# Kernel optimization log

Measured on AMD Instinct MI355X. Metric: run time of the kernel, lower is better.

Reference implementation:

```python
import jax, jax.numpy as jnp
import numpy as np
import math

B, N, CS = 1, 2048, 384
H, C, PQK, PV = 12, 16, 4, 8
INF, EPS = 100000.0, 1e-08


def setup_inputs() -> dict:
    key = jax.random.key(0)
    ks = jax.random.split(key, 16)
    hc = H * C
    hpq = H * PQK * 3
    hpkv = H * (PQK + PV) * 3
    cod = H * (C + 4 * PV)
    sc = 0.02
    return {
        "s": jax.random.normal(ks[0], (B, N, CS), jnp.float32),
        "rot": jax.random.normal(ks[1], (B, N, 3, 3), jnp.float32),
        "trans": jax.random.normal(ks[2], (B, N, 3), jnp.float32),
        "mask": jnp.ones((B, N), jnp.float32),
        "Wq": jax.random.normal(ks[3], (hc, CS), jnp.float32) * sc,
        "bq": jnp.zeros((hc,), jnp.float32),
        "Wkv": jax.random.normal(ks[4], (2 * hc, CS), jnp.float32) * sc,
        "bkv": jnp.zeros((2 * hc,), jnp.float32),
        "Wqp": jax.random.normal(ks[5], (hpq, CS), jnp.float32) * sc,
        "bqp": jnp.zeros((hpq,), jnp.float32),
        "Wkvp": jax.random.normal(ks[6], (hpkv, CS), jnp.float32) * sc,
        "bkvp": jnp.zeros((hpkv,), jnp.float32),
        "head_weights": jnp.full((H,), 0.541324854612918, jnp.float32),
        "Wout": jax.random.normal(ks[7], (CS, H * cod // H), jnp.float32) * sc,
        "bout": jnp.zeros((CS,), jnp.float32),
    }


def _points(s, W, b, rot, trans, npts):
    # torch.split into 3 chunks of H*npts then stack at -1 -> [B,N,H*npts,3]
    p = jnp.einsum("bni,oi->bno", s, W) + b
    p = jnp.moveaxis(p.reshape(B, N, 3, H * npts), -2, -1)  # [B,N,H*npts,3]
    p = jnp.einsum("bnij,bnmj->bnmi", rot, p) + trans[:, :, None, :]  # rigid apply
    return p.reshape(B, N, H, npts, 3)


def reference(s, rot, trans, mask, Wq, bq, Wkv, bkv, Wqp, bqp, Wkvp, bkvp, head_weights, Wout, bout):
    q = (jnp.einsum("bni,oi->bno", s, Wq) + bq).reshape(B, N, H, C)
    kv = (jnp.einsum("bni,oi->bno", s, Wkv) + bkv).reshape(B, N, H, 2 * C)
    k, v = kv[..., :C], kv[..., C:]

    q_pts = _points(s, Wqp, bqp, rot, trans, PQK)             # [B,N,H,PQK,3]
    kv_pts = _points(s, Wkvp, bkvp, rot, trans, PQK + PV)
    k_pts, v_pts = kv_pts[..., :PQK, :], kv_pts[..., PQK:, :]  # [B,N,H,PQK,3], [B,N,H,PV,3]

    a = jnp.einsum("bihc,bjhc->bhij", q, k) * math.sqrt(1.0 / (3 * C))

    # sum_{p,c} |q_pts_i - k_pts_j|^2 via norm expansion (avoids [N,N,P,3])
    q2 = jnp.moveaxis(jnp.sum(q_pts ** 2, axis=(-1, -2)), -1, 1)  # [B,H,N]
    k2 = jnp.moveaxis(jnp.sum(k_pts ** 2, axis=(-1, -2)), -1, 1)
    cross = jnp.einsum("bihpc,bjhpc->bhij", q_pts, k_pts)
    d2 = q2[..., :, None] + k2[..., None, :] - 2.0 * cross       # [B,H,N,N]

    hw = jax.nn.softplus(head_weights) * math.sqrt(1.0 / (3 * (PQK * 9.0 / 2)))
    pt_att = -0.5 * hw[None, :, None, None] * d2

    sq_mask = INF * (mask[:, None, :, None] * mask[:, None, None, :] - 1.0)  # [B,1,N,N]
    a = jax.nn.softmax(a + pt_att + sq_mask, axis=-1)

    o = jnp.einsum("bhij,bjhc->bihc", a, v).reshape(B, N, H * C)
    o_pt = jnp.einsum("bhij,bjhpc->bihpc", a, v_pts)             # [B,N,H,PV,3]
    o_pt = jnp.einsum("bnji,bnhpj->bnhpi", rot, o_pt - trans[:, :, None, None, :])  # invert_apply

    dists = jnp.sqrt(jnp.sum(o_pt ** 2, axis=-1) + EPS).reshape(B, N, H * PV)
    o_pt_f = o_pt.reshape(B, N, H * PV, 3)
    feats = jnp.concatenate([o, o_pt_f[..., 0], o_pt_f[..., 1], o_pt_f[..., 2], dists], axis=-1)
    return jnp.einsum("bnf,of->bno", feats, Wout) + bout
```

## Files before the change

### kernel.cpp

```cpp
#include <hip/hip_runtime.h>
#include <hip/hip_bf16.h>
#include <cstdint>
#include <cstddef>

#define Hh    12
#define Nseq  2048
#define PSTR  1152
#define EPSm  1e-8f
#define MASKV 1024.0f

typedef unsigned short ushort_t;
typedef __attribute__((ext_vector_type(8))) short bf8_t;
typedef __attribute__((ext_vector_type(4))) short s4_t;
typedef __attribute__((ext_vector_type(4))) float f4_t;

#define OFF_PALL   0
#define OFF_WALLB  2359296
#define OFF_BALL   2580480
#define OFF_SB     2581632
#define OFF_WOUTB  2974848
#define OFF_FEATSB 3085440
#define OFF_AU     3675264
#define OFF_KU     4068480
#define OFF_VU     4461696
#define WS_FLOATS  5051520

__device__ __forceinline__ ushort_t bfr(float x) {
    union { float f; uint32_t u; } v; v.f = x;
    uint32_t r = v.u + 0x7FFFu + ((v.u >> 16) & 1u);
    return (ushort_t)(r >> 16);
}

__global__ __launch_bounds__(256) void prep(
    const float* __restrict__ s, const float* __restrict__ Wout,
    const float* __restrict__ Wq, const float* __restrict__ Wkv,
    const float* __restrict__ Wqp, const float* __restrict__ Wkvp,
    const float* __restrict__ bq, const float* __restrict__ bkv,
    const float* __restrict__ bqp, const float* __restrict__ bkvp,
    ushort_t* __restrict__ Wallb, float* __restrict__ ball,
    ushort_t* __restrict__ sb, ushort_t* __restrict__ Woutb)
{
    int idx = blockIdx.x * 256 + threadIdx.x;
    if (idx < 1152 * 384) {
        int r = idx / 384, c = idx % 384;
        float v;
        if (r < 192)      v = Wq [(size_t)r * 384 + c];
        else if (r < 576) v = Wkv[(size_t)(r - 192) * 384 + c];
        else if (r < 720) v = Wqp[(size_t)(r - 576) * 384 + c];
        else              v = Wkvp[(size_t)(r - 720) * 384 + c];
        Wallb[idx] = bfr(v);
    }
    if (idx < 1152) {
        float v;
        if (idx < 192)      v = bq[idx];
        else if (idx < 576) v = bkv[idx - 192];
        else if (idx < 720) v = bqp[idx - 576];
        else                v = bkvp[idx - 720];
        ball[idx] = v;
    }
    if (idx < 2048 * 384) sb[idx] = bfr(s[idx]);
    if (idx < 384 * 576)  Woutb[idx] = bfr(Wout[idx]);
}

template<int BM, int BN>
__global__ __launch_bounds__(256) void gemm_mfma(
    const ushort_t* __restrict__ A, const ushort_t* __restrict__ W,
    const float* __restrict__ bias, float* __restrict__ C,
    int M, int Nn, int K)
{
    constexpr int WM = BM / 2, WN = BN / 2;
    constexpr int MI = WM / 16, NJ = WN / 16;
    __shared__ ushort_t As[BM][40];
    __shared__ ushort_t Bs[BN][40];

    const int bm = blockIdx.y * BM;
    const int bn = blockIdx.x * BN;
    const int t  = threadIdx.x;
    const int w  = t >> 6, lane = t & 63;
    const int m  = lane & 15, quad = lane >> 4;
    const int wm = (w >> 1) * WM, wn = (w & 1) * WN;

    f4_t acc[MI][NJ];
    #pragma unroll
    for (int i2 = 0; i2 < MI; ++i2)
        #pragma unroll
        for (int j2 = 0; j2 < NJ; ++j2)
            acc[i2][j2] = (f4_t){0.f, 0.f, 0.f, 0.f};

    for (int k0 = 0; k0 < K; k0 += 32) {
        #pragma unroll
        for (int u = 0; u < BM / 64; ++u) {
            int e = t + u * 256;
            int r = e >> 2, kk = (e & 3) * 8;
            *(uint4*)&As[r][kk] = *(const uint4*)&A[(size_t)(bm + r) * K + k0 + kk];
        }
        #pragma unroll
        for (int u = 0; u < BN / 64; ++u) {
            int e = t + u * 256;
            int r = e >> 2, kk = (e & 3) * 8;
            *(uint4*)&Bs[r][kk] = *(const uint4*)&W[(size_t)(bn + r) * K + k0 + kk];
        }
        __syncthreads();
        bf8_t af[MI], bfv[NJ];
        #pragma unroll
        for (int x = 0; x < MI; ++x) af[x]  = *(const bf8_t*)&As[wm + x * 16 + m][quad * 8];
        #pragma unroll
        for (int x = 0; x < NJ; ++x) bfv[x] = *(const bf8_t*)&Bs[wn + x * 16 + m][quad * 8];
        #pragma unroll
        for (int i2 = 0; i2 < MI; ++i2)
            #pragma unroll
            for (int j2 = 0; j2 < NJ; ++j2)
                acc[i2][j2] = __builtin_amdgcn_mfma_f32_16x16x32_bf16(
                    af[i2], bfv[j2], acc[i2][j2], 0, 0, 0);
        __syncthreads();
    }

    #pragma unroll
    for (int j2 = 0; j2 < NJ; ++j2) {
        int col = bn + wn + j2 * 16 + m;
        float bb = bias[col];
        #pragma unroll
        for (int i2 = 0; i2 < MI; ++i2)
            #pragma unroll
            for (int r = 0; r < 4; ++r) {
                int row = bm + wm + i2 * 16 + quad * 4 + r;
                C[(size_t)row * Nn + col] = acc[i2][j2][r] + bb;
            }
    }
}

__global__ __launch_bounds__(128) void pack_aug(
    const float* __restrict__ Pall, const float* __restrict__ rot,
    const float* __restrict__ trans, const float* __restrict__ mask,
    const float* __restrict__ hwv,
    ushort_t* __restrict__ AU, ushort_t* __restrict__ KU,
    ushort_t* __restrict__ VU)
{
    __shared__ float S[8][1156];
    const int n0 = blockIdx.x * 8;
    const int t  = threadIdx.x;

    #pragma unroll
    for (int u = 0; u < 18; ++u) {
        int f = t + u * 128;
        int rr = f / 288, c4 = f % 288;
        float4 v = *(const float4*)&Pall[(size_t)(n0 + rr) * PSTR + c4 * 4];
        *(float4*)&S[rr][c4 * 4] = v;
    }
    __syncthreads();

    if (t >= 96) return;
    const int nl = t & 7, h = t >> 3;
    const int n  = n0 + nl;
    const float* row = S[nl];

    const float whw = 0.5f * logf(1.0f + expf(hwv[h])) * 0.13608276348795434f;
    const float scale_a = 0.14433756729740643f;

    float R[9], T[3];
    #pragma unroll
    for (int z = 0; z < 9; ++z) R[z] = rot[(size_t)n * 9 + z];
    #pragma unroll
    for (int d = 0; d < 3; ++d) T[d] = trans[(size_t)n * 3 + d];

    float qpv[12], q2 = 0.f;
    #pragma unroll
    for (int p = 0; p < 4; ++p) {
        float r0 = row[576 +   0 + h * 4 + p];
        float r1 = row[576 +  48 + h * 4 + p];
        float r2 = row[576 +  96 + h * 4 + p];
        #pragma unroll
        for (int d = 0; d < 3; ++d) {
            float o = R[d*3+0]*r0 + R[d*3+1]*r1 + R[d*3+2]*r2 + T[d];
            qpv[p * 3 + d] = o;
            q2 += o * o;
        }
    }

    float kpv[12], vpv[24], k2 = 0.f;
    #pragma unroll
    for (int pt = 0; pt < 12; ++pt) {
        float r0 = row[720 +   0 + h * 12 + pt];
        float r1 = row[720 + 144 + h * 12 + pt];
        float r2 = row[720 + 288 + h * 12 + pt];
        #pragma unroll
        for (int d = 0; d < 3; ++d) {
            float o = R[d*3+0]*r0 + R[d*3+1]*r1 + R[d*3+2]*r2 + T[d];
            if (pt < 4) { kpv[pt * 3 + d] = o; k2 += o * o; }
            else        { vpv[(pt - 4) * 3 + d] = o; }
        }
    }

    const float mi = mask[n];

    __align__(16) ushort_t a32[32];
    #pragma unroll
    for (int c = 0; c < 16; ++c) a32[c] = bfr(row[h * 16 + c] * scale_a);
    #pragma unroll
    for (int z = 0; z < 12; ++z) a32[16 + z] = bfr(qpv[z] * (2.0f * whw));
    a32[28] = bfr(-whw);
    a32[29] = bfr(-whw * q2);
    a32[30] = bfr(mi * MASKV);
    a32[31] = bfr(-MASKV);
    ushort_t* adst = AU + ((size_t)h * Nseq + n) * 32;
    #pragma unroll
    for (int u = 0; u < 4; ++u) ((uint4*)adst)[u] = ((const uint4*)a32)[u];

    const float* kvrow = row + 192 + h * 32;
    __align__(16) ushort_t k32[32];
    #pragma unroll
    for (int c = 0; c < 16; ++c) k32[c] = bfr(kvrow[c]);
    #pragma unroll
    for (int z = 0; z < 12; ++z) k32[16 + z] = bfr(kpv[z]);
    k32[28] = bfr(k2);
    k32[29] = 0x3F80;
    k32[30] = bfr(mi);
    k32[31] = 0x3F80;
    ushort_t* kdst = KU + ((size_t)h * Nseq + n) * 32;
    #pragma unroll
    for (int u = 0; u < 4; ++u) ((uint4*)kdst)[u] = ((const uint4*)k32)[u];

    ushort_t* vb = VU + (size_t)h * 98304 + (size_t)(n >> 5) * 1536 + (n & 31);
    #pragma unroll
    for (int c = 0; c < 16; ++c) vb[c * 32] = bfr(kvrow[16 + c]);
    #pragma unroll
    for (int z = 0; z < 24; ++z) vb[(16 + z) * 32] = bfr(vpv[z]);
    vb[40 * 32] = 0x3F80;
    #pragma unroll
    for (int c = 41; c < 48; ++c) vb[c * 32] = 0;
}

__device__ __forceinline__ bf8_t expack(f4_t s) {
    s4_t p;
    p[0] = (short)bfr(__expf(s[0]));
    p[1] = (short)bfr(__expf(s[1]));
    p[2] = (short)bfr(__expf(s[2]));
    p[3] = (short)bfr(__expf(s[3]));
    s4_t z = (s4_t)0;
    return __builtin_shufflevector(p, z, 0, 1, 2, 3, 4, 5, 6, 7);
}

__device__ __forceinline__ bf8_t vpad(s4_t v) {
    s4_t z = (s4_t)0;
    return __builtin_shufflevector(v, z, 0, 1, 2, 3, 4, 5, 6, 7);
}

struct KVTile { bf8_t kb0, kb1; s4_t v[6]; };

__device__ __forceinline__ KVTile load_tile(
    const ushort_t* __restrict__ kb_base, const ushort_t* __restrict__ vt,
    int m, int quad)
{
    KVTile tl;
    tl.kb0  = *(const bf8_t*)(kb_base);
    tl.kb1  = *(const bf8_t*)(kb_base + 16 * 32);
    tl.v[0] = *(const s4_t*)(vt +        m * 32 +      quad * 4);
    tl.v[1] = *(const s4_t*)(vt +  512 + m * 32 +      quad * 4);
    tl.v[2] = *(const s4_t*)(vt + 1024 + m * 32 +      quad * 4);
    tl.v[3] = *(const s4_t*)(vt +        m * 32 + 16 + quad * 4);
    tl.v[4] = *(const s4_t*)(vt +  512 + m * 32 + 16 + quad * 4);
    tl.v[5] = *(const s4_t*)(vt + 1024 + m * 32 + 16 + quad * 4);
    return tl;
}

__global__ __launch_bounds__(256, 3) void attn_mfma(
    const ushort_t* __restrict__ AU, const ushort_t* __restrict__ KU,
    const ushort_t* __restrict__ VU,
    const float* __restrict__ rot, const float* __restrict__ trans,
    ushort_t* __restrict__ featsb)
{
    __shared__ float red[4][32][49];

    const int b    = blockIdx.x;
    const int h    = b >> 6;
    const int ib   = b & 63;
    const int t    = threadIdx.x;
    const int w    = t >> 6;
    const int lane = t & 63;
    const int m    = lane & 15;
    const int quad = lane >> 4;
    const int i0   = ib * 32;

    bf8_t afA = *(const bf8_t*)(AU + ((size_t)h * Nseq + i0 +      m) * 32 + quad * 8);
    bf8_t afB = *(const bf8_t*)(AU + ((size_t)h * Nseq + i0 + 16 + m) * 32 + quad * 8);

    f4_t acc[6];
    #pragma unroll
    for (int z = 0; z < 6; ++z) acc[z] = (f4_t){0.f, 0.f, 0.f, 0.f};

    const int jb0 = w * 512;
    const ushort_t* kb_base = KU + ((size_t)h * Nseq + jb0 + m) * 32 + quad * 8;
    const ushort_t* v_base  = VU + (size_t)h * 98304 + (size_t)jb0 * 48;

    KVTile cur = load_tile(kb_base, v_base, m, quad);

    #pragma unroll
    for (int jt = 0; jt < 16; ++jt) {
        f4_t zz = (f4_t){0.f, 0.f, 0.f, 0.f};
        f4_t sXA = __builtin_amdgcn_mfma_f32_16x16x32_bf16(cur.kb0, afA, zz, 0, 0, 0);
        f4_t sXB = __builtin_amdgcn_mfma_f32_16x16x32_bf16(cur.kb0, afB, zz, 0, 0, 0);
        f4_t sYA = __builtin_amdgcn_mfma_f32_16x16x32_bf16(cur.kb1, afA, zz, 0, 0, 0);
        f4_t sYB = __builtin_amdgcn_mfma_f32_16x16x32_bf16(cur.kb1, afB, zz, 0, 0, 0);

        KVTile nxt;
        if (jt < 15)
            nxt = load_tile(kb_base + (size_t)(jt + 1) * 32 * 32,
                            v_base + (size_t)(jt + 1) * 1536, m, quad);

        bf8_t pXA = expack(sXA), pXB = expack(sXB);
        bf8_t pYA = expack(sYA), pYB = expack(sYB);
        bf8_t f0 = vpad(cur.v[0]), f1 = vpad(cur.v[1]), f2 = vpad(cur.v[2]);
        bf8_t g0 = vpad(cur.v[3]), g1 = vpad(cur.v[4]), g2 = vpad(cur.v[5]);

        acc[0] = __builtin_amdgcn_mfma_f32_16x16x32_bf16(pXA, f0, acc[0], 0, 0, 0);
        acc[0] = __builtin_amdgcn_mfma_f32_16x16x32_bf16(pYA, g0, acc[0], 0, 0, 0);
        acc[1] = __builtin_amdgcn_mfma_f32_16x16x32_bf16(pXA, f1, acc[1], 0, 0, 0);
        acc[1] = __builtin_amdgcn_mfma_f32_16x16x32_bf16(pYA, g1, acc[1], 0, 0, 0);
        acc[2] = __builtin_amdgcn_mfma_f32_16x16x32_bf16(pXA, f2, acc[2], 0, 0, 0);
        acc[2] = __builtin_amdgcn_mfma_f32_16x16x32_bf16(pYA, g2, acc[2], 0, 0, 0);
        acc[3] = __builtin_amdgcn_mfma_f32_16x16x32_bf16(pXB, f0, acc[3], 0, 0, 0);
        acc[3] = __builtin_amdgcn_mfma_f32_16x16x32_bf16(pYB, g0, acc[3], 0, 0, 0);
        acc[4] = __builtin_amdgcn_mfma_f32_16x16x32_bf16(pXB, f1, acc[4], 0, 0, 0);
        acc[4] = __builtin_amdgcn_mfma_f32_16x16x32_bf16(pYB, g1, acc[4], 0, 0, 0);
        acc[5] = __builtin_amdgcn_mfma_f32_16x16x32_bf16(pXB, f2, acc[5], 0, 0, 0);
        acc[5] = __builtin_amdgcn_mfma_f32_16x16x32_bf16(pYB, g2, acc[5], 0, 0, 0);

        cur = nxt;
    }

    #pragma unroll
    for (int r = 0; r < 4; ++r) {
        red[w][quad * 4 + r][m]           = acc[0][r];
        red[w][quad * 4 + r][16 + m]      = acc[1][r];
        red[w][quad * 4 + r][32 + m]      = acc[2][r];
        red[w][16 + quad * 4 + r][m]      = acc[3][r];
        red[w][16 + quad * 4 + r][16 + m] = acc[4][r];
        red[w][16 + quad * 4 + r][32 + m] = acc[5][r];
    }
    __syncthreads();

    #pragma unroll
    for (int u = 0; u < 6; ++u) {
        int e = t + u * 256;
        int rr = e / 48, cc = e % 48;
        red[0][rr][cc] = red[0][rr][cc] + red[1][rr][cc] + red[2][rr][cc] + red[3][rr][cc];
    }
    __syncthreads();

    if (t < 32) {
        const int i = i0 + t;
        float L   = red[0][t][40];
        float inv = 1.0f / L;
        float o[40];
        #pragma unroll
        for (int z = 0; z < 40; ++z) o[z] = red[0][t][z] * inv;

        ushort_t* f = featsb + (size_t)i * 576;
        #pragma unroll
        for (int c = 0; c < 16; ++c) f[h * 16 + c] = bfr(o[c]);

        float R[9], T[3];
        #pragma unroll
        for (int z = 0; z < 9; ++z) R[z] = rot[(size_t)i * 9 + z];
        #pragma unroll
        for (int d = 0; d < 3; ++d) T[d] = trans[(size_t)i * 3 + d];

        #pragma unroll
        for (int p8 = 0; p8 < 8; ++p8) {
            float g0 = o[16 + p8 * 3 + 0] - T[0];
            float g1 = o[16 + p8 * 3 + 1] - T[1];
            float g2 = o[16 + p8 * 3 + 2] - T[2];
            float xx = R[0] * g0 + R[3] * g1 + R[6] * g2;
            float yy = R[1] * g0 + R[4] * g1 + R[7] * g2;
            float zz = R[2] * g0 + R[5] * g1 + R[8] * g2;
            float dist = sqrtf(xx * xx + yy * yy + zz * zz + EPSm);
            f[192 + h * 8 + p8] = bfr(xx);
            f[288 + h * 8 + p8] = bfr(yy);
            f[384 + h * 8 + p8] = bfr(zz);
            f[480 + h * 8 + p8] = bfr(dist);
        }
    }
}

extern "C" void kernel_launch(void* const* d_in, const int* in_sizes, int n_in,
                              void* d_out, int out_size, void* d_ws, size_t ws_size,
                              hipStream_t stream)
{
    const float* s     = (const float*)d_in[0];
    const float* rot   = (const float*)d_in[1];
    const float* trans = (const float*)d_in[2];
    const float* mask  = (const float*)d_in[3];
    const float* Wq    = (const float*)d_in[4];
    const float* bq    = (const float*)d_in[5];
    const float* Wkv   = (const float*)d_in[6];
    const float* bkv   = (const float*)d_in[7];
    const float* Wqp   = (const float*)d_in[8];
    const float* bqp   = (const float*)d_in[9];
    const float* Wkvp  = (const float*)d_in[10];
    const float* bkvp  = (const float*)d_in[11];
    const float* hwv   = (const float*)d_in[12];
    const float* Wout  = (const float*)d_in[13];
    const float* bout  = (const float*)d_in[14];
    float* out = (float*)d_out;
    float* ws  = (float*)d_ws;

    if (ws_size < (size_t)WS_FLOATS * sizeof(float)) return;

    float*    Pall   = ws + OFF_PALL;
    ushort_t* Wallb  = (ushort_t*)(ws + OFF_WALLB);
    float*    ball   = ws + OFF_BALL;
    ushort_t* sb     = (ushort_t*)(ws + OFF_SB);
    ushort_t* Woutb  = (ushort_t*)(ws + OFF_WOUTB);
    ushort_t* featsb = (ushort_t*)(ws + OFF_FEATSB);
    ushort_t* AU     = (ushort_t*)(ws + OFF_AU);
    ushort_t* KU     = (ushort_t*)(ws + OFF_KU);
    ushort_t* VU     = (ushort_t*)(ws + OFF_VU);

    prep<<<dim3(3072), 256, 0, stream>>>(s, Wout, Wq, Wkv, Wqp, Wkvp,
                                         bq, bkv, bqp, bkvp,
                                         Wallb, ball, sb, Woutb);

    gemm_mfma<128, 64><<<dim3(1152 / 64, 2048 / 128), 256, 0, stream>>>(
        sb, Wallb, ball, Pall, 2048, 1152, 384);

    pack_aug<<<dim3(256), 128, 0, stream>>>(Pall, rot, trans, mask, hwv,
                                            AU, KU, VU);

    attn_mfma<<<dim3(768), 256, 0, stream>>>(AU, KU, VU, rot, trans, featsb);

    gemm_mfma<64, 64><<<dim3(384 / 64, 2048 / 64), 256, 0, stream>>>(
        featsb, Woutb, bout, out, 2048, 384, 576);
}
```

Measured before the change: 139.8 us.

## Retile attention to 64 query rows with split-KV partials and finalize kernel

The attention kernel now handles 64 query rows per block instead of 32. The key range is split into two halves across blocks, so each K/V tile loaded is reused across four A fragments, and the per-wave key range is halved. Unnormalized partial sums go to two fp32 workspace buffers, and a new attn_fin kernel combines them, normalizes, and applies the inverse rigid transform. The projection GEMM tile also shrinks from 128x64 to 64x64 to give more blocks. The cost is an extra kernel launch, partial-sum traffic to global memory, a larger LDS reduction buffer, and more accumulator registers under the 3-blocks-per-SM launch bound.

```diff
diff --git a/kernel.cpp b/kernel.cpp
--- a/kernel.cpp
+++ b/kernel.cpp
@@ -23,7 +23,9 @@
 #define OFF_AU     3675264
 #define OFF_KU     4068480
 #define OFF_VU     4461696
-#define WS_FLOATS  5051520
+#define OFF_P0     5051520
+#define OFF_P1     6059136
+#define WS_FLOATS  7066752
 
 __device__ __forceinline__ ushort_t bfr(float x) {
     union { float f; uint32_t u; } v; v.f = x;
@@ -266,119 +268,134 @@
 __global__ __launch_bounds__(256, 3) void attn_mfma(
     const ushort_t* __restrict__ AU, const ushort_t* __restrict__ KU,
     const ushort_t* __restrict__ VU,
-    const float* __restrict__ rot, const float* __restrict__ trans,
-    ushort_t* __restrict__ featsb)
-{
-    __shared__ float red[4][32][49];
+    float* __restrict__ part0, float* __restrict__ part1)
+{
+    __shared__ float red[4][64][49];
 
     const int b    = blockIdx.x;
     const int h    = b >> 6;
-    const int ib   = b & 63;
+    const int r6   = b & 63;
+    const int ib   = r6 >> 1;
+    const int jh   = r6 & 1;
     const int t    = threadIdx.x;
     const int w    = t >> 6;
     const int lane = t & 63;
     const int m    = lane & 15;
     const int quad = lane >> 4;
-    const int i0   = ib * 32;
-
-    bf8_t afA = *(const bf8_t*)(AU + ((size_t)h * Nseq + i0 +      m) * 32 + quad * 8);
-    bf8_t afB = *(const bf8_t*)(AU + ((size_t)h * Nseq + i0 + 16 + m) * 32 + quad * 8);
-
-    f4_t acc[6];
-    #pragma unroll
-    for (int z = 0; z < 6; ++z) acc[z] = (f4_t){0.f, 0.f, 0.f, 0.f};
-
-    const int jb0 = w * 512;
-    const ushort_t* kb_base = KU + ((size_t)h * Nseq + jb0 + m) * 32 + quad * 8;
-    const ushort_t* v_base  = VU + (size_t)h * 98304 + (size_t)jb0 * 48;
+    const int i0   = ib * 64;
+
+    bf8_t af[4];
+    #pragma unroll
+    for (int x = 0; x < 4; ++x)
+        af[x] = *(const bf8_t*)(AU + ((size_t)h * Nseq + i0 + x * 16 + m) * 32 + quad * 8);
+
+    f4_t acc[12];
+    #pragma unroll
+    for (int z = 0; z < 12; ++z) acc[z] = (f4_t){0.f, 0.f, 0.f, 0.f};
+
+    const int jbeg = jh * 1024 + w * 256;
+    const ushort_t* kb_base = KU + ((size_t)h * Nseq + jbeg + m) * 32 + quad * 8;
+    const ushort_t* v_base  = VU + (size_t)h * 98304 + (size_t)jbeg * 48;
 
     KVTile cur = load_tile(kb_base, v_base, m, quad);
 
     #pragma unroll
-    for (int jt = 0; jt < 16; ++jt) {
-        f4_t zz = (f4_t){0.f, 0.f, 0.f, 0.f};
-        f4_t sXA = __builtin_amdgcn_mfma_f32_16x16x32_bf16(cur.kb0, afA, zz, 0, 0, 0);
-        f4_t sXB = __builtin_amdgcn_mfma_f32_16x16x32_bf16(cur.kb0, afB, zz, 0, 0, 0);
-        f4_t sYA = __builtin_amdgcn_mfma_f32_16x16x32_bf16(cur.kb1, afA, zz, 0, 0, 0);
-        f4_t sYB = __builtin_amdgcn_mfma_f32_16x16x32_bf16(cur.kb1, afB, zz, 0, 0, 0);
-
+    for (int jt = 0; jt < 8; ++jt) {
         KVTile nxt;
-        if (jt < 15)
-            nxt = load_tile(kb_base + (size_t)(jt + 1) * 32 * 32,
+        if (jt < 7)
+            nxt = load_tile(kb_base + (size_t)(jt + 1) * 1024,
                             v_base + (size_t)(jt + 1) * 1536, m, quad);
 
-        bf8_t pXA = expack(sXA), pXB = expack(sXB);
-        bf8_t pYA = expack(sYA), pYB = expack(sYB);
         bf8_t f0 = vpad(cur.v[0]), f1 = vpad(cur.v[1]), f2 = vpad(cur.v[2]);
         bf8_t g0 = vpad(cur.v[3]), g1 = vpad(cur.v[4]), g2 = vpad(cur.v[5]);
-
-        acc[0] = __builtin_amdgcn_mfma_f32_16x16x32_bf16(pXA, f0, acc[0], 0, 0, 0);
-        acc[0] = __builtin_amdgcn_mfma_f32_16x16x32_bf16(pYA, g0, acc[0], 0, 0, 0);
-        acc[1] = __builtin_amdgcn_mfma_f32_16x16x32_bf16(pXA, f1, acc[1], 0, 0, 0);
-        acc[1] = __builtin_amdgcn_mfma_f32_16x16x32_bf16(pYA, g1, acc[1], 0, 0, 0);
-        acc[2] = __builtin_amdgcn_mfma_f32_16x16x32_bf16(pXA, f2, acc[2], 0, 0, 0);
-        acc[2] = __builtin_amdgcn_mfma_f32_16x16x32_bf16(pYA, g2, acc[2], 0, 0, 0);
-        acc[3] = __builtin_amdgcn_mfma_f32_16x16x32_bf16(pXB, f0, acc[3], 0, 0, 0);
-        acc[3] = __builtin_amdgcn_mfma_f32_16x16x32_bf16(pYB, g0, acc[3], 0, 0, 0);
-        acc[4] = __builtin_amdgcn_mfma_f32_16x16x32_bf16(pXB, f1, acc[4], 0, 0, 0);
-        acc[4] = __builtin_amdgcn_mfma_f32_16x16x32_bf16(pYB, g1, acc[4], 0, 0, 0);
-        acc[5] = __builtin_amdgcn_mfma_f32_16x16x32_bf16(pXB, f2, acc[5], 0, 0, 0);
-        acc[5] = __builtin_amdgcn_mfma_f32_16x16x32_bf16(pYB, g2, acc[5], 0, 0, 0);
-
+        f4_t zz = (f4_t){0.f, 0.f, 0.f, 0.f};
+
+        #pragma unroll
+        for (int x = 0; x < 4; ++x) {
+            f4_t sX = __builtin_amdgcn_mfma_f32_16x16x32_bf16(cur.kb0, af[x], zz, 0, 0, 0);
+            f4_t sY = __builtin_amdgcn_mfma_f32_16x16x32_bf16(cur.kb1, af[x], zz, 0, 0, 0);
+            bf8_t pX = expack(sX);
+            bf8_t pY = expack(sY);
+            acc[x*3+0] = __builtin_amdgcn_mfma_f32_16x16x32_bf16(pX, f0, acc[x*3+0], 0, 0, 0);
+            acc[x*3+0] = __builtin_amdgcn_mfma_f32_16x16x32_bf16(pY, g0, acc[x*3+0], 0, 0, 0);
+            acc[x*3+1] = __builtin_amdgcn_mfma_f32_16x16x32_bf16(pX, f1, acc[x*3+1], 0, 0, 0);
+            acc[x*3+1] = __builtin_amdgcn_mfma_f32_16x16x32_bf16(pY, g1, acc[x*3+1], 0, 0, 0);
+            acc[x*3+2] = __builtin_amdgcn_mfma_f32_16x16x32_bf16(pX, f2, acc[x*3+2], 0, 0, 0);
+            acc[x*3+2] = __builtin_amdgcn_mfma_f32_16x16x32_bf16(pY, g2, acc[x*3+2], 0, 0, 0);
+        }
         cur = nxt;
     }
 
     #pragma unroll
-    for (int r = 0; r < 4; ++r) {
-        red[w][quad * 4 + r][m]           = acc[0][r];
-        red[w][quad * 4 + r][16 + m]      = acc[1][r];
-        red[w][quad * 4 + r][32 + m]      = acc[2][r];
-        red[w][16 + quad * 4 + r][m]      = acc[3][r];
-        red[w][16 + quad * 4 + r][16 + m] = acc[4][r];
-        red[w][16 + quad * 4 + r][32 + m] = acc[5][r];
-    }
+    for (int x = 0; x < 4; ++x)
+        #pragma unroll
+        for (int r = 0; r < 4; ++r) {
+            red[w][x * 16 + quad * 4 + r][m]      = acc[x*3+0][r];
+            red[w][x * 16 + quad * 4 + r][16 + m] = acc[x*3+1][r];
+            red[w][x * 16 + quad * 4 + r][32 + m] = acc[x*3+2][r];
+        }
     __syncthreads();
 
     #pragma unroll
-    for (int u = 0; u < 6; ++u) {
+    for (int u = 0; u < 12; ++u) {
         int e = t + u * 256;
         int rr = e / 48, cc = e % 48;
         red[0][rr][cc] = red[0][rr][cc] + red[1][rr][cc] + red[2][rr][cc] + red[3][rr][cc];
     }
     __syncthreads();
 
-    if (t < 32) {
-        const int i = i0 + t;
-        float L   = red[0][t][40];
-        float inv = 1.0f / L;
-        float o[40];
-        #pragma unroll
-        for (int z = 0; z < 40; ++z) o[z] = red[0][t][z] * inv;
-
-        ushort_t* f = featsb + (size_t)i * 576;
-        #pragma unroll
-        for (int c = 0; c < 16; ++c) f[h * 16 + c] = bfr(o[c]);
-
-        float R[9], T[3];
-        #pragma unroll
-        for (int z = 0; z < 9; ++z) R[z] = rot[(size_t)i * 9 + z];
-        #pragma unroll
-        for (int d = 0; d < 3; ++d) T[d] = trans[(size_t)i * 3 + d];
-
-        #pragma unroll
-        for (int p8 = 0; p8 < 8; ++p8) {
-            float g0 = o[16 + p8 * 3 + 0] - T[0];
-            float g1 = o[16 + p8 * 3 + 1] - T[1];
-            float g2 = o[16 + p8 * 3 + 2] - T[2];
-            float xx = R[0] * g0 + R[3] * g1 + R[6] * g2;
-            float yy = R[1] * g0 + R[4] * g1 + R[7] * g2;
-            float zz = R[2] * g0 + R[5] * g1 + R[8] * g2;
-            float dist = sqrtf(xx * xx + yy * yy + zz * zz + EPSm);
-            f[192 + h * 8 + p8] = bfr(xx);
-            f[288 + h * 8 + p8] = bfr(yy);
-            f[384 + h * 8 + p8] = bfr(zz);
-            f[480 + h * 8 + p8] = bfr(dist);
-        }
+    float* dst = (jh ? part1 : part0) + ((size_t)h * Nseq + i0) * 41;
+    #pragma unroll
+    for (int u = 0; u < 11; ++u) {
+        int e = t + u * 256;
+        if (e < 2624) {
+            int rr = e / 41, cc = e % 41;
+            dst[(size_t)rr * 41 + cc] = red[0][rr][cc];
+        }
+    }
+}
+
+__global__ __launch_bounds__(256) void attn_fin(
+    const float* __restrict__ part0, const float* __restrict__ part1,
+    const float* __restrict__ rot, const float* __restrict__ trans,
+    ushort_t* __restrict__ featsb)
+{
+    int idx = blockIdx.x * 256 + threadIdx.x;
+    if (idx >= Nseq * Hh) return;
+    int i = idx / Hh, h = idx % Hh;
+
+    const float* a = part0 + ((size_t)h * Nseq + i) * 41;
+    const float* bb = part1 + ((size_t)h * Nseq + i) * 41;
+
+    float L = a[40] + bb[40];
+    float inv = 1.0f / L;
+    float o[40];
+    #pragma unroll
+    for (int z = 0; z < 40; ++z) o[z] = (a[z] + bb[z]) * inv;
+
+    ushort_t* f = featsb + (size_t)i * 576;
+    #pragma unroll
+    for (int c = 0; c < 16; ++c) f[h * 16 + c] = bfr(o[c]);
+
+    float R[9], T[3];
+    #pragma unroll
+    for (int z = 0; z < 9; ++z) R[z] = rot[(size_t)i * 9 + z];
+    #pragma unroll
+    for (int d = 0; d < 3; ++d) T[d] = trans[(size_t)i * 3 + d];
+
+    #pragma unroll
+    for (int p8 = 0; p8 < 8; ++p8) {
+        float g0 = o[16 + p8 * 3 + 0] - T[0];
+        float g1 = o[16 + p8 * 3 + 1] - T[1];
+        float g2 = o[16 + p8 * 3 + 2] - T[2];
+        float xx = R[0] * g0 + R[3] * g1 + R[6] * g2;
+        float yy = R[1] * g0 + R[4] * g1 + R[7] * g2;
+        float zz = R[2] * g0 + R[5] * g1 + R[8] * g2;
+        float dist = sqrtf(xx * xx + yy * yy + zz * zz + EPSm);
+        f[192 + h * 8 + p8] = bfr(xx);
+        f[288 + h * 8 + p8] = bfr(yy);
+        f[384 + h * 8 + p8] = bfr(zz);
+        f[480 + h * 8 + p8] = bfr(dist);
     }
 }
 
@@ -415,18 +432,22 @@
     ushort_t* AU     = (ushort_t*)(ws + OFF_AU);
     ushort_t* KU     = (ushort_t*)(ws + OFF_KU);
     ushort_t* VU     = (ushort_t*)(ws + OFF_VU);
+    float*    part0  = ws + OFF_P0;
+    float*    part1  = ws + OFF_P1;
 
     prep<<<dim3(3072), 256, 0, stream>>>(s, Wout, Wq, Wkv, Wqp, Wkvp,
                                          bq, bkv, bqp, bkvp,
                                          Wallb, ball, sb, Woutb);
 
-    gemm_mfma<128, 64><<<dim3(1152 / 64, 2048 / 128), 256, 0, stream>>>(
+    gemm_mfma<64, 64><<<dim3(1152 / 64, 2048 / 64), 256, 0, stream>>>(
         sb, Wallb, ball, Pall, 2048, 1152, 384);
 
     pack_aug<<<dim3(256), 128, 0, stream>>>(Pall, rot, trans, mask, hwv,
                                             AU, KU, VU);
 
-    attn_mfma<<<dim3(768), 256, 0, stream>>>(AU, KU, VU, rot, trans, featsb);
+    attn_mfma<<<dim3(768), 256, 0, stream>>>(AU, KU, VU, part0, part1);
+
+    attn_fin<<<dim3(96), 256, 0, stream>>>(part0, part1, rot, trans, featsb);
 
     gemm_mfma<64, 64><<<dim3(384 / 64, 2048 / 64), 256, 0, stream>>>(
         featsb, Woutb, bout, out, 2048, 384, 576);
```

After: 138.0 us. Within noise of the previous version (-1.3%).
